# Optimization experiments

Hardware: AMD Instinct MI355X
Metric: run time of the kernel (lower is better)

Reference implementation:

```python
import jax, jax.numpy as jnp
import numpy as np

DEPTH = 3  # args.depth (chemprop default)


def setup_inputs() -> dict:
    key = jax.random.key(0)
    ks = jax.random.split(key, 10)
    n_atoms, n_bonds, max_nb, n_mols = 100000, 200000, 6, 4000
    H, AF, BF = 300, 133, 147  # hidden_size, atom_fdim, bond_fdim

    f_atoms = jax.random.normal(ks[0], (n_atoms, AF), jnp.float32)
    f_bonds = jax.random.normal(ks[1], (n_bonds, BF), jnp.float32)
    a2b = jax.random.randint(ks[2], (n_atoms, max_nb), 0, n_bonds)      # incoming bonds per atom
    b2a = jax.random.randint(ks[3], (n_bonds,), 0, n_atoms)             # source atom per bond
    b2revb = jax.random.randint(ks[4], (n_bonds,), 0, n_bonds)          # reverse bond index
    atom_mol = jnp.sort(jax.random.randint(ks[5], (n_atoms,), 0, n_mols))  # contiguous mol segments (a_scope)

    # Learned params (W_i, W_h bias-free per args.bias=False; W_o has bias)
    W_i = jax.random.normal(ks[6], (BF, H), jnp.float32) * (1.0 / np.sqrt(BF))
    W_h = jax.random.normal(ks[7], (H, H), jnp.float32) * (1.0 / np.sqrt(H))
    W_o = jax.random.normal(ks[8], (AF + H, H), jnp.float32) * (1.0 / np.sqrt(AF + H))
    b_o = jax.random.normal(ks[9], (H,), jnp.float32) * 0.01

    return dict(f_atoms=f_atoms, f_bonds=f_bonds, W_i=W_i, W_h=W_h, W_o=W_o, b_o=b_o,
                a2b=a2b, b2a=b2a, b2revb=b2revb, atom_mol=atom_mol, n_mols=n_mols)


def reference(f_atoms, f_bonds, W_i, W_h, W_o, b_o, a2b, b2a, b2revb, atom_mol, n_mols):
    # Bond-message D-MPNN (atom_messages=False), ReLU activation, dropout=0 (eval)
    inp = f_bonds @ W_i                       # [n_bonds, H]
    message = jax.nn.relu(inp)
    for _ in range(DEPTH - 1):
        nei_a_message = message[a2b]          # [n_atoms, max_nb, H] gather
        a_message = nei_a_message.sum(axis=1) # [n_atoms, H]
        message = a_message[b2a] - message[b2revb]  # [n_bonds, H]
        message = jax.nn.relu(inp + message @ W_h)
    # Atom readout
    a_message = message[a2b].sum(axis=1)      # [n_atoms, H]
    a_input = jnp.concatenate([f_atoms, a_message], axis=1)
    atom_hiddens = jax.nn.relu(a_input @ W_o + b_o)  # [n_atoms, H]
    # Per-molecule mean aggregation (a_scope loop -> segment ops)
    sums = jax.ops.segment_sum(atom_hiddens, atom_mol, num_segments=n_mols)
    counts = jax.ops.segment_sum(jnp.ones((atom_hiddens.shape[0],), atom_hiddens.dtype),
                                 atom_mol, num_segments=n_mols)
    return sums / jnp.maximum(counts, 1.0)[:, None]  # empty mols -> zero vector
```

## Files before the change

kernel.cpp:

```cpp
#include <hip/hip_runtime.h>
#include <hip/hip_bf16.h>
#include <stdint.h>


#define H_DIM 300
#define HP 320
#define AF_DIM 133
#define BF_DIM 147
#define MAXNB 6

typedef __hip_bfloat16 bf16;
typedef __attribute__((ext_vector_type(8))) short short8;
typedef __attribute__((ext_vector_type(4))) float f32x4;

__device__ __forceinline__ float b2f_raw(unsigned short u) {
    union { unsigned int i; float f; } v; v.i = ((unsigned int)u) << 16; return v.f;
}
__device__ __forceinline__ unsigned short f2b_raw(float f) {
    union { float f; unsigned int i; } v; v.f = f;
    unsigned int x = v.i;
    x += 0x7fffu + ((x >> 16) & 1u);
    return (unsigned short)(x >> 16);
}

__global__ __launch_bounds__(256) void prep_wt(
    const float* __restrict__ s1, int r1,
    const float* __restrict__ s2, int r2,
    unsigned short* __restrict__ Wt, int nkt)
{
    const int Ktot = nkt * 32;
    const int idx = blockIdx.x * 256 + threadIdx.x;
    if (idx >= 320 * Ktot) return;
    const int n = idx % 320;
    const int k = idx / 320;
    float v = 0.f;
    if (n < H_DIM) {
        if (k < 320) { if (k < r1) v = s1[k * H_DIM + n]; }
        else { const int kk = k - 320; if (kk < r2) v = s2[kk * H_DIM + n]; }
    }
    Wt[n * Ktot + k] = f2b_raw(v);
}

__global__ __launch_bounds__(256) void prep_cvt(
    const float* __restrict__ in, int W,
    unsigned short* __restrict__ outb, int ostride, int M)
{
    const int idx = blockIdx.x * 256 + threadIdx.x;
    if (idx >= M * 20) return;
    const int r = idx / 20;
    const int cc = idx - r * 20;
    uint4 o;
    unsigned short* op = (unsigned short*)&o;
#pragma unroll
    for (int j = 0; j < 8; ++j) {
        const int k = cc * 8 + j;
        op[j] = (k < W) ? f2b_raw(in[(long)r * W + k]) : 0;
    }
    *(uint4*)(outb + (long)r * ostride + cc * 8) = o;
}

template <int NKT, int ASTR, bool RELU_A, bool BIAS_RELU>
__global__ __launch_bounds__(256) void mfma_gemm(
    const unsigned short* __restrict__ Ab,
    const unsigned short* __restrict__ Wt,
    const float* __restrict__ bias,
    bf16* __restrict__ out,
    int M)
{
    constexpr int KTOT = NKT * 32;

    __shared__ char Cs[16 * 640];

    const int t    = threadIdx.x;
    const int m0   = blockIdx.x * 64;
    const int wc   = t >> 6;
    const int lane = t & 63;
    const int l16  = lane & 15;
    const int quad = lane >> 4;

    long arow[4];
#pragma unroll
    for (int mt = 0; mt < 4; ++mt)
        arow[mt] = (long)min(m0 + mt * 16 + l16, M - 1) * ASTR + quad * 8;

    auto load_a = [&](int kt, short8* afr) {
#pragma unroll
        for (int mt = 0; mt < 4; ++mt) {
            short8 v = *(const short8*)(Ab + arow[mt] + kt * 32);
            if (RELU_A) {
                unsigned short* rp = (unsigned short*)&v;
#pragma unroll
                for (int j = 0; j < 8; ++j)
                    rp[j] = (rp[j] & 0x8000u) ? 0 : rp[j];
            }
            afr[mt] = v;
        }
    };

    auto load_b = [&](int kt, short8* bfr) {
        const int kbase = kt * 32 + quad * 8;
#pragma unroll
        for (int nt = 0; nt < 5; ++nt) {
            const int nn = wc * 80 + nt * 16 + l16;
            bfr[nt] = *(const short8*)(Wt + (long)nn * KTOT + kbase);
        }
    };

    f32x4 acc[4][5];
#pragma unroll
    for (int i = 0; i < 4; ++i)
#pragma unroll
        for (int j = 0; j < 5; ++j) acc[i][j] = (f32x4){0.f, 0.f, 0.f, 0.f};

    short8 afr[4], bfr[5], afr_n[4], bfr_n[5];
    load_a(0, afr);
    load_b(0, bfr);

    for (int kt = 0; kt < NKT; ++kt) {
        if (kt + 1 < NKT) {
            load_a(kt + 1, afr_n);
            load_b(kt + 1, bfr_n);
        }
#pragma unroll
        for (int nt = 0; nt < 5; ++nt)
#pragma unroll
            for (int mt = 0; mt < 4; ++mt)
                acc[mt][nt] = __builtin_amdgcn_mfma_f32_16x16x32_bf16(
                    afr[mt], bfr[nt], acc[mt][nt], 0, 0, 0);
        if (kt + 1 < NKT) {
#pragma unroll
            for (int mt = 0; mt < 4; ++mt) afr[mt] = afr_n[mt];
#pragma unroll
            for (int nt = 0; nt < 5; ++nt) bfr[nt] = bfr_n[nt];
        }
    }

    for (int mt = 0; mt < 4; ++mt) {
        __syncthreads();
#pragma unroll
        for (int nt = 0; nt < 5; ++nt) {
            const int col = wc * 80 + nt * 16 + l16;
            float bv = 0.f;
            if (BIAS_RELU) bv = (col < H_DIM) ? bias[col] : 0.f;
#pragma unroll
            for (int r = 0; r < 4; ++r) {
                float v = acc[mt][nt][r] + bv;
                if (BIAS_RELU) v = fmaxf(v, 0.f);
                ((unsigned short*)Cs)[(quad * 4 + r) * HP + col] = f2b_raw(v);
            }
        }
        __syncthreads();
        const int gr0 = m0 + mt * 16;
#pragma unroll
        for (int i = 0; i < 3; ++i) {
            const int idx = i * 256 + t;
            if (idx < 640) {
                const int row = idx / 40;
                if (gr0 + row < M)
                    *(uint4*)((char*)out + (long)(gr0 + row) * 640 + (idx - row * 40) * 16)
                        = *(const uint4*)(Cs + idx * 16);
            }
        }
    }
}

__global__ __launch_bounds__(256) void gather_sum_kernel(
    const bf16* __restrict__ msg, const int* __restrict__ a2b,
    unsigned short* __restrict__ amsg, int ostride, int n_atoms)
{
    const int idx = blockIdx.x * 256 + threadIdx.x;
    if (idx >= n_atoms * (HP / 8)) return;
    const int a = idx / (HP / 8);
    const int cc = idx - a * (HP / 8);
    float s[8] = {0.f, 0.f, 0.f, 0.f, 0.f, 0.f, 0.f, 0.f};
    const int base = a * MAXNB;
#pragma unroll
    for (int j = 0; j < MAXNB; ++j) {
        const long b = a2b[base + j];
        const uint4 u = *(const uint4*)((const char*)msg + (b * HP + cc * 8) * 2);
        const unsigned short* up = (const unsigned short*)&u;
#pragma unroll
        for (int e = 0; e < 8; ++e) s[e] += b2f_raw(up[e]);
    }
    uint4 r;
    unsigned short* rp = (unsigned short*)&r;
#pragma unroll
    for (int e = 0; e < 8; ++e) rp[e] = f2b_raw(s[e]);
    *(uint4*)(amsg + (long)a * ostride + cc * 8) = r;
}

__global__ __launch_bounds__(256) void combine_kernel(
    const bf16* __restrict__ inp, const bf16* __restrict__ Gh,
    const bf16* __restrict__ Hm, const int* __restrict__ b2a,
    const int* __restrict__ b2revb, bf16* __restrict__ outm, int n_bonds)
{
    const int idx = blockIdx.x * 256 + threadIdx.x;
    if (idx >= n_bonds * (HP / 8)) return;
    const int b = idx / (HP / 8);
    const int cc = idx - b * (HP / 8);
    const long co = (long)cc * 16;
    const long ra = b2a[b];
    const long rb = b2revb[b];
    const uint4 vi = *(const uint4*)((const char*)inp + (long)b * 640 + co);
    const uint4 vg = *(const uint4*)((const char*)Gh + ra * 640 + co);
    const uint4 vh = *(const uint4*)((const char*)Hm + rb * 640 + co);
    const unsigned short* ip = (const unsigned short*)&vi;
    const unsigned short* gp = (const unsigned short*)&vg;
    const unsigned short* hp = (const unsigned short*)&vh;
    uint4 r;
    unsigned short* rp = (unsigned short*)&r;
#pragma unroll
    for (int e = 0; e < 8; ++e) {
        const float v = b2f_raw(ip[e]) + b2f_raw(gp[e]) - b2f_raw(hp[e]);
        rp[e] = f2b_raw(fmaxf(v, 0.f));
    }
    *(uint4*)((char*)outm + (long)b * 640 + co) = r;
}

__global__ __launch_bounds__(256) void seg_mean_kernel(
    const bf16* __restrict__ hidden, const int* __restrict__ atom_mol,
    float* __restrict__ out, int n_atoms)
{
    const int m = blockIdx.x;
    __shared__ int s_lo, s_hi;
    if (threadIdx.x == 0) {
        int lo = 0, hi = n_atoms;
        while (lo < hi) { int mid = (lo + hi) >> 1; if (atom_mol[mid] < m) lo = mid + 1; else hi = mid; }
        s_lo = lo;
        int lo2 = lo; hi = n_atoms;
        while (lo2 < hi) { int mid = (lo2 + hi) >> 1; if (atom_mol[mid] < m + 1) lo2 = mid + 1; else hi = mid; }
        s_hi = lo2;
    }
    __syncthreads();
    const int lo = s_lo, hi = s_hi;
    const float inv = 1.0f / (float)max(hi - lo, 1);
    for (int cpass = 0; cpass < 2; ++cpass) {
        const int c = cpass * 256 + threadIdx.x;
        if (c >= H_DIM) break;
        float s = 0.f;
        for (int a = lo; a < hi; ++a)
            s += b2f_raw(((const unsigned short*)hidden)[(long)a * HP + c]);
        out[(long)m * H_DIM + c] = s * inv;
    }
}

extern "C" void kernel_launch(void* const* d_in, const int* in_sizes, int n_in,
                              void* d_out, int out_size, void* d_ws, size_t ws_size,
                              hipStream_t stream)
{
    const float* f_atoms = (const float*)d_in[0];
    const float* f_bonds = (const float*)d_in[1];
    const float* W_i     = (const float*)d_in[2];
    const float* W_h     = (const float*)d_in[3];
    const float* W_o     = (const float*)d_in[4];
    const float* b_o     = (const float*)d_in[5];
    const int*  a2b      = (const int*)d_in[6];
    const int*  b2a      = (const int*)d_in[7];
    const int*  b2revb   = (const int*)d_in[8];
    const int*  atom_mol = (const int*)d_in[9];

    const int n_atoms = in_sizes[0] / AF_DIM;
    const int n_bonds = in_sizes[1] / BF_DIM;
    const int n_mols  = out_size / H_DIM;

    char* ws = (char*)d_ws;
    size_t off = 0;
    auto alloc = [&](size_t bytes) {
        size_t o = off; off += (bytes + 255) & ~(size_t)255; return o;
    };
    bf16* inpB = (bf16*)(ws + alloc((size_t)n_bonds * HP * 2));
    bf16* msgX = (bf16*)(ws + alloc((size_t)n_bonds * HP * 2));
    bf16* HmB  = (bf16*)(ws + alloc((size_t)n_bonds * HP * 2));
    bf16* amsg = (bf16*)(ws + alloc((size_t)n_atoms * HP * 2));
    unsigned short* Wt1 = (unsigned short*)(ws + alloc(320 * 160 * 2));
    unsigned short* WtH = (unsigned short*)(ws + alloc(320 * 320 * 2));
    unsigned short* Wt3 = (unsigned short*)(ws + alloc(320 * 480 * 2));
    unsigned short* fb16    = (unsigned short*)HmB;
    unsigned short* atomcat = (unsigned short*)inpB;
    bf16* hidden = HmB;

    const dim3 blk(256);

    prep_wt<<<(320 * 160 + 255) / 256, blk, 0, stream>>>(W_i, BF_DIM, nullptr, 0, Wt1, 5);
    prep_wt<<<(320 * 320 + 255) / 256, blk, 0, stream>>>(W_h, H_DIM, nullptr, 0, WtH, 10);
    prep_wt<<<(320 * 480 + 255) / 256, blk, 0, stream>>>(W_o + (size_t)AF_DIM * H_DIM, H_DIM,
                                                         W_o, AF_DIM, Wt3, 15);

    const int gB = (n_bonds + 63) / 64;
    const int gA = (n_atoms + 63) / 64;
    const int gG = (n_atoms * (HP / 8) + 255) / 256;
    const int gC = (n_bonds * (HP / 8) + 255) / 256;

    prep_cvt<<<(n_bonds * 20 + 255) / 256, blk, 0, stream>>>(f_bonds, BF_DIM, fb16, 160, n_bonds);

    mfma_gemm<5, 160, false, false><<<gB, blk, 0, stream>>>(fb16, Wt1, nullptr, inpB, n_bonds);

    mfma_gemm<10, 320, true, false><<<gB, blk, 0, stream>>>(
        (const unsigned short*)inpB, WtH, nullptr, HmB, n_bonds);
    gather_sum_kernel<<<gG, blk, 0, stream>>>(HmB, a2b, (unsigned short*)amsg, HP, n_atoms);
    combine_kernel<<<gC, blk, 0, stream>>>(inpB, amsg, HmB, b2a, b2revb, msgX, n_bonds);

    mfma_gemm<10, 320, false, false><<<gB, blk, 0, stream>>>(
        (const unsigned short*)msgX, WtH, nullptr, HmB, n_bonds);
    gather_sum_kernel<<<gG, blk, 0, stream>>>(HmB, a2b, (unsigned short*)amsg, HP, n_atoms);
    combine_kernel<<<gC, blk, 0, stream>>>(inpB, amsg, HmB, b2a, b2revb, msgX, n_bonds);

    prep_cvt<<<(n_atoms * 20 + 255) / 256, blk, 0, stream>>>(f_atoms, AF_DIM, atomcat + 320, 480, n_atoms);
    gather_sum_kernel<<<gG, blk, 0, stream>>>(msgX, a2b, atomcat, 480, n_atoms);
    mfma_gemm<15, 480, false, true><<<gA, blk, 0, stream>>>(atomcat, Wt3, b_o, hidden, n_atoms);

    seg_mean_kernel<<<n_mols, blk, 0, stream>>>(hidden, atom_mol, (float*)d_out, n_atoms);
}
```

Baseline: 1.101 ms.

## Stage A tiles through LDS with async global_load_lds double buffering

The GEMM kernel used to have each of the four waves load its own copy of the 64-row A tile from global memory into registers. Now the block loads the A tile once into a double-buffered LDS region using global_load_lds, and each wave reads its fragments from LDS. This cuts redundant global A traffic by a factor of four. In exchange it adds a __syncthreads per k-step and drops the register prefetch of B, which could expose B load latency.

```diff
diff --git a/kernel.cpp b/kernel.cpp
--- a/kernel.cpp
+++ b/kernel.cpp
@@ -21,6 +21,13 @@
     unsigned int x = v.i;
     x += 0x7fffu + ((x >> 16) & 1u);
     return (unsigned short)(x >> 16);
+}
+
+__device__ __forceinline__ void gload16(const void* g, void* l) {
+    __builtin_amdgcn_global_load_lds(
+        (const __attribute__((address_space(1))) unsigned int*)g,
+        (__attribute__((address_space(3))) unsigned int*)l,
+        16, 0, 0);
 }
 
 __global__ __launch_bounds__(256) void prep_wt(
@@ -69,6 +76,7 @@
 {
     constexpr int KTOT = NKT * 32;
 
+    __shared__ char As[2][64 * 64];
     __shared__ char Cs[16 * 640];
 
     const int t    = threadIdx.x;
@@ -78,15 +86,40 @@
     const int l16  = lane & 15;
     const int quad = lane >> 4;
 
-    long arow[4];
-#pragma unroll
-    for (int mt = 0; mt < 4; ++mt)
-        arow[mt] = (long)min(m0 + mt * 16 + l16, M - 1) * ASTR + quad * 8;
-
-    auto load_a = [&](int kt, short8* afr) {
+    const int am = t >> 2;
+    const int c  = t & 3;
+    const int gm = min(m0 + am, M - 1);
+    const unsigned short* const agp = Ab + (long)gm * ASTR + c * 8;
+    char* const lds0 = As[0] + t * 16;
+    char* const lds1 = As[1] + t * 16;
+
+    auto load_b = [&](int kt, short8* bfr) {
+        const int kbase = kt * 32 + quad * 8;
+#pragma unroll
+        for (int nt = 0; nt < 5; ++nt) {
+            const int nn = wc * 80 + nt * 16 + l16;
+            bfr[nt] = *(const short8*)(Wt + (long)nn * KTOT + kbase);
+        }
+    };
+
+    f32x4 acc[4][5];
+#pragma unroll
+    for (int i = 0; i < 4; ++i)
+#pragma unroll
+        for (int j = 0; j < 5; ++j) acc[i][j] = (f32x4){0.f, 0.f, 0.f, 0.f};
+
+    gload16(agp, lds0);
+    __syncthreads();
+
+    for (int kt = 0; kt < NKT; ++kt) {
+        short8 bfr[5];
+        load_b(kt, bfr);
+        if (kt + 1 < NKT)
+            gload16(agp + (kt + 1) * 32, ((kt + 1) & 1) ? lds1 : lds0);
+        short8 afr[4];
 #pragma unroll
         for (int mt = 0; mt < 4; ++mt) {
-            short8 v = *(const short8*)(Ab + arow[mt] + kt * 32);
+            short8 v = *(const short8*)(As[kt & 1] + (mt * 16 + l16) * 64 + quad * 16);
             if (RELU_A) {
                 unsigned short* rp = (unsigned short*)&v;
 #pragma unroll
@@ -95,44 +128,13 @@
             }
             afr[mt] = v;
         }
-    };
-
-    auto load_b = [&](int kt, short8* bfr) {
-        const int kbase = kt * 32 + quad * 8;
-#pragma unroll
-        for (int nt = 0; nt < 5; ++nt) {
-            const int nn = wc * 80 + nt * 16 + l16;
-            bfr[nt] = *(const short8*)(Wt + (long)nn * KTOT + kbase);
-        }
-    };
-
-    f32x4 acc[4][5];
-#pragma unroll
-    for (int i = 0; i < 4; ++i)
-#pragma unroll
-        for (int j = 0; j < 5; ++j) acc[i][j] = (f32x4){0.f, 0.f, 0.f, 0.f};
-
-    short8 afr[4], bfr[5], afr_n[4], bfr_n[5];
-    load_a(0, afr);
-    load_b(0, bfr);
-
-    for (int kt = 0; kt < NKT; ++kt) {
-        if (kt + 1 < NKT) {
-            load_a(kt + 1, afr_n);
-            load_b(kt + 1, bfr_n);
-        }
 #pragma unroll
         for (int nt = 0; nt < 5; ++nt)
 #pragma unroll
             for (int mt = 0; mt < 4; ++mt)
                 acc[mt][nt] = __builtin_amdgcn_mfma_f32_16x16x32_bf16(
                     afr[mt], bfr[nt], acc[mt][nt], 0, 0, 0);
-        if (kt + 1 < NKT) {
-#pragma unroll
-            for (int mt = 0; mt < 4; ++mt) afr[mt] = afr_n[mt];
-#pragma unroll
-            for (int nt = 0; nt < 5; ++nt) bfr[nt] = bfr_n[nt];
-        }
+        __syncthreads();
     }
 
     for (int mt = 0; mt < 4; ++mt) {
```

Result: faster. 1.040 ms (-5.5%).
